# Performance work log

Hardware: AMD Instinct MI355X
Metric: run time of the kernel (lower is better)

Reference implementation:

```python
import jax, jax.numpy as jnp
import numpy as np

# ThrusterLagConfig constants
PWM_CENTER = 7.5
PWM_HALF_RANGE = 2.5
DEADZONE = 0.05
SAT_GAIN = 2.0
TAU_INIT = 0.08
TAU_MIN = 0.01
DT = 0.01
N_THRUSTERS = 8


def setup_inputs() -> dict:
    key = jax.random.key(0)
    k_u, = jax.random.split(key, 1)
    B, L, C = 512, 8192, N_THRUSTERS
    # raw PWM duty in [5, 10]
    u_seq = jax.random.uniform(k_u, (B, L, C), dtype=jnp.float32, minval=5.0, maxval=10.0)
    # learnable tau parameter, initialized as in __init__:
    # tau0 = clamp(tau_init - tau_min, 1e-6); p0 = log(expm1(tau0))
    tau0 = max(TAU_INIT - TAU_MIN, 1e-6)
    p0 = float(np.log(np.expm1(tau0)))
    tau_param = jnp.full((C,), p0, dtype=jnp.float32)
    return {"u_seq": u_seq, "tau_param": tau_param}


def reference(u_seq, tau_param):
    # PWM duty -> [-1, 1]
    u_unit = (u_seq - PWM_CENTER) / PWM_HALF_RANGE
    # deadzone: softshrink(u, lambd) = sign(u) * max(|u| - lambd, 0)
    u_dz = jnp.sign(u_unit) * jnp.maximum(jnp.abs(u_unit) - DEADZONE, 0.0)
    # smooth saturation
    u_nl = jnp.tanh(SAT_GAIN * u_dz)  # (B, L, C)

    # a = exp(-dt / tau), tau = softplus(p) + tau_min, per channel (C,)
    tau = jax.nn.softplus(tau_param) + TAU_MIN
    a = jnp.exp(-DT / tau)  # (C,)

    # first-order lag IIR: u_eff[k] = a * u_eff[k-1] + (1 - a) * u_nl[k]
    # u0_eff defaults to u_nl[:, 0, :]
    u0 = u_nl[:, 0, :]  # (B, C)

    def step(u_prev, uk):
        u_new = a * u_prev + (1.0 - a) * uk
        return u_new, u_new

    xs = jnp.moveaxis(u_nl, 1, 0)  # (L, B, C)
    _, ys = jax.lax.scan(step, u0, xs)
    return jnp.moveaxis(ys, 0, 1)  # (B, L, C)
```

## Files before the change

kernel.cpp:

```cpp
#include <hip/hip_runtime.h>
#include <math.h>


typedef float v4f __attribute__((ext_vector_type(4)));

constexpr int kB     = 512;
constexpr int kL     = 8192;
constexpr int kC     = 8;
constexpr int kOut   = 512;
constexpr int kChunk = 128;
constexpr int kSegs  = kL / kOut;

constexpr float kDT     = 0.01f;
constexpr float kTauMin = 0.01f;

__device__ __forceinline__ float rfl(float x) {
    return __int_as_float(__builtin_amdgcn_readfirstlane(__float_as_int(x)));
}

__device__ __forceinline__ float softplus_f(float p) {
    return fmaxf(p, 0.0f) + log1pf(__expf(-fabsf(p)));
}

__device__ __forceinline__ v4f u_nl4(v4f u) {
    v4f s = u * 0.8f - 6.0f;
    v4f x;
    #pragma unroll
    for (int i = 0; i < 4; ++i) {
        float cl = fminf(fmaxf(s[i], -0.1f), 0.1f);
        x[i] = s[i] - cl;
    }
    v4f t = x * x;
    v4f p = t * -0.0072811f + 0.070674f;
    p = t * p - 0.297221f;
    p = t * p + 0.996226f;
    return x * p;
}

template<int CTRL>
__device__ __forceinline__ float dpp_mov(float v) {
    return __int_as_float(__builtin_amdgcn_update_dpp(
        0, __float_as_int(v), CTRL, 0xF, 0xF, false));
}
#define DPP_SHR(d)   (0x110 | (d))
#define DPP_BC15     0x142
#define DPP_BC31     0x143

__device__ __forceinline__ float bperm(int addr, float v) {
    return __int_as_float(__builtin_amdgcn_ds_bpermute(addr, __float_as_int(v)));
}

#define PROC(X0, X1, X2, X3, CH, DO_PF, DO_ST)                                  \
    {                                                                           \
        v4f n0 = u_nl4(X0), n1 = u_nl4(X1), n2 = u_nl4(X2), n3 = u_nl4(X3);     \
        if (DO_PF) {                                                            \
            const float* nb = base +                                            \
                (size_t)(start + ((CH) + 2) * kChunk + lane * 2) * kC;          \
            X0 = *(const v4f*)(nb);                                             \
            X1 = *(const v4f*)(nb + 4);                                         \
            X2 = *(const v4f*)(nb + 8);                                         \
            X3 = *(const v4f*)(nb + 12);                                        \
        }                                                                       \
        v4f l00 = O0 * n0;                                                      \
        v4f l01 = O1 * n1;                                                      \
        v4f l10 = A0 * l00 + O0 * n2;                                           \
        v4f l11 = A1 * l01 + O1 * n3;                                           \
        float I[kC];                                                            \
        for (int c = 0; c < 4; ++c) { I[c] = l10[c]; I[c + 4] = l11[c]; }       \
        for (int c = 0; c < kC; ++c)                                            \
            I[c] = fmaf(a2[c], dpp_mov<DPP_SHR(1)>(I[c]), I[c]);                \
        for (int c = 0; c < kC; ++c)                                            \
            I[c] = fmaf(a4[c], dpp_mov<DPP_SHR(2)>(I[c]), I[c]);                \
        for (int c = 0; c < kC; ++c)                                            \
            I[c] = fmaf(a8[c], dpp_mov<DPP_SHR(4)>(I[c]), I[c]);                \
        for (int c = 0; c < kC; ++c)                                            \
            I[c] = fmaf(a16[c], dpp_mov<DPP_SHR(8)>(I[c]), I[c]);               \
        for (int c = 0; c < 4; ++c) {                                           \
            I[c]     = fmaf(W15a[c], dpp_mov<DPP_BC15>(I[c]),     I[c]);        \
            I[c + 4] = fmaf(W15b[c], dpp_mov<DPP_BC15>(I[c + 4]), I[c + 4]);    \
        }                                                                       \
        for (int c = 0; c < 4; ++c) {                                           \
            I[c]     = fmaf(W31a[c], dpp_mov<DPP_BC31>(I[c]),     I[c]);        \
            I[c + 4] = fmaf(W31b[c], dpp_mov<DPP_BC31>(I[c + 4]), I[c + 4]);    \
        }                                                                       \
        v4f Tt0, Tt1;                                                           \
        for (int c = 0; c < 4; ++c) {                                           \
            Tt0[c] = bperm(addr63, I[c]);                                       \
            Tt1[c] = bperm(addr63, I[c + 4]);                                   \
        }                                                                       \
        v4f I0 = {I[0], I[1], I[2], I[3]};                                      \
        v4f I1 = {I[4], I[5], I[6], I[7]};                                      \
        v4f E0 = (I0 - l10) * V0;                                               \
        v4f E1 = (I1 - l11) * V1;                                               \
        if (DO_ST) {                                                            \
            float* ob = obase +                                                 \
                (size_t)(start + (CH) * kChunk + lane * 2) * kC;                \
            v4f C0  = D0 * K0 + E0;                                             \
            v4f C1  = D1 * K1 + E1;                                             \
            v4f cy0 = A0 * C0;                                                  \
            v4f cy1 = A1 * C1;                                                  \
            *(v4f*)(ob)      = l00 + cy0;                                       \
            *(v4f*)(ob + 4)  = l01 + cy1;                                       \
            *(v4f*)(ob + 8)  = A0 * cy0 + l10;                                  \
            *(v4f*)(ob + 12) = A1 * cy1 + l11;                                  \
        }                                                                       \
        K0 = M0 * K0 + Tt0;                                                     \
        K1 = M1 * K1 + Tt1;                                                     \
    }

__global__ __launch_bounds__(256, 2) void scan_seg(const float* __restrict__ u,
                                                   const float* __restrict__ tp,
                                                   float* __restrict__ out) {
    const int lane = threadIdx.x & 63;
    const int seg  = blockIdx.x * 4 + (threadIdx.x >> 6);
    const int r    = seg >> 4;
    const int sq   = seg & (kSegs - 1);

    float a2[kC], a4[kC], a8[kC], a16[kC];
    float a[kC], om[kC], ia2[kC], Ms[kC];
    v4f D0, D1, W15a, W15b, W31a, W31b;
    #pragma unroll
    for (int c = 0; c < kC; ++c) {
        float tau = softplus_f(tp[c]) + kTauMin;
        float lna = -kDT / tau;
        float av  = __expf(lna);
        float v2 = av * av, v4 = v2 * v2, v8 = v4 * v4;
        a[c]   = rfl(av);
        om[c]  = rfl(1.0f - av);
        a2[c]  = rfl(v2);
        a4[c]  = rfl(v4);
        a8[c]  = rfl(v8);
        a16[c] = rfl(v8 * v8);
        ia2[c] = rfl(1.0f / v2);
        Ms[c]  = rfl(__expf(lna * (float)kChunk));
        float d   = __expf(lna * (float)(2 * lane));
        float w15 = (lane & 16)  ? __expf(lna * (float)(2 * ((lane & 15) + 1))) : 0.0f;
        float w31 = (lane >= 32) ? __expf(lna * (float)(2 * (lane - 31)))       : 0.0f;
        if (c < 4) { D0[c] = d; W15a[c] = w15; W31a[c] = w31; }
        else       { D1[c-4] = d; W15b[c-4] = w15; W31b[c-4] = w31; }
    }
    v4f A0 = {a[0],a[1],a[2],a[3]},     A1 = {a[4],a[5],a[6],a[7]};
    v4f O0 = {om[0],om[1],om[2],om[3]}, O1 = {om[4],om[5],om[6],om[7]};
    v4f V0 = {ia2[0],ia2[1],ia2[2],ia2[3]}, V1 = {ia2[4],ia2[5],ia2[6],ia2[7]};
    v4f M0 = {Ms[0],Ms[1],Ms[2],Ms[3]}, M1 = {Ms[4],Ms[5],Ms[6],Ms[7]};

    const float* base  = u   + (size_t)r * kL * kC;
    float*       obase = out + (size_t)r * kL * kC;

    const int addr63 = 63 << 2;

    v4f K0, K1;
    int start;
    if (sq == 0) {
        start = 0;
        K0 = u_nl4(*(const v4f*)(base));
        K1 = u_nl4(*(const v4f*)(base + 4));
    } else {
        start = sq * kOut - kChunk;
        K0 = (v4f){0, 0, 0, 0};
        K1 = (v4f){0, 0, 0, 0};
    }

    const float* pA = base + (size_t)(start + lane * 2) * kC;
    const float* pB = pA + (size_t)kChunk * kC;
    v4f xa0 = *(const v4f*)(pA);
    v4f xa1 = *(const v4f*)(pA + 4);
    v4f xa2 = *(const v4f*)(pA + 8);
    v4f xa3 = *(const v4f*)(pA + 12);
    v4f xb0 = *(const v4f*)(pB);
    v4f xb1 = *(const v4f*)(pB + 4);
    v4f xb2 = *(const v4f*)(pB + 8);
    v4f xb3 = *(const v4f*)(pB + 12);

    if (sq == 0) {
        PROC(xa0, xa1, xa2, xa3, 0, true,  true);
        PROC(xb0, xb1, xb2, xb3, 1, true,  true);
        PROC(xa0, xa1, xa2, xa3, 2, false, true);
        PROC(xb0, xb1, xb2, xb3, 3, false, true);
    } else {
        PROC(xa0, xa1, xa2, xa3, 0, true,  false);
        PROC(xb0, xb1, xb2, xb3, 1, true,  true);
        PROC(xa0, xa1, xa2, xa3, 2, true,  true);
        PROC(xb0, xb1, xb2, xb3, 3, false, true);
        PROC(xa0, xa1, xa2, xa3, 4, false, true);
    }
}

extern "C" void kernel_launch(void* const* d_in, const int* in_sizes, int n_in,
                              void* d_out, int out_size, void* d_ws, size_t ws_size,
                              hipStream_t stream) {
    const float* u  = (const float*)d_in[0];
    const float* tp = (const float*)d_in[1];
    float* out = (float*)d_out;

    scan_seg<<<(kB * kSegs) / 4, 256, 0, stream>>>(u, tp, out);
}
```

Before: 57.45 us.

## Software-pipeline chunk scans ahead of dependent stores and carry updates

Splits the per-chunk processing into a scan phase, a store phase and a carry-update phase. The scan of the next chunk is interleaved ahead of the previous chunk's store, so the DPP/bpermute scan work overlaps the serial carry chain. It also drops the launch_bounds occupancy hint. Keeping two chunks of intermediates live raises register pressure, and without the bound the compiler may pick lower occupancy.

```diff
diff --git a/kernel.cpp b/kernel.cpp
--- a/kernel.cpp
+++ b/kernel.cpp
@@ -50,23 +50,23 @@
     return __int_as_float(__builtin_amdgcn_ds_bpermute(addr, __float_as_int(v)));
 }
 
-#define PROC(X0, X1, X2, X3, CH, DO_PF, DO_ST)                                  \
+#define SCANM(l00v, l01v, l10v, l11v, E0v, E1v, T0v, T1v, X0, X1, X2, X3, DO_PF, PFCH) \
     {                                                                           \
         v4f n0 = u_nl4(X0), n1 = u_nl4(X1), n2 = u_nl4(X2), n3 = u_nl4(X3);     \
         if (DO_PF) {                                                            \
             const float* nb = base +                                            \
-                (size_t)(start + ((CH) + 2) * kChunk + lane * 2) * kC;          \
+                (size_t)(start + (PFCH) * kChunk + lane * 2) * kC;              \
             X0 = *(const v4f*)(nb);                                             \
             X1 = *(const v4f*)(nb + 4);                                         \
             X2 = *(const v4f*)(nb + 8);                                         \
             X3 = *(const v4f*)(nb + 12);                                        \
         }                                                                       \
-        v4f l00 = O0 * n0;                                                      \
-        v4f l01 = O1 * n1;                                                      \
-        v4f l10 = A0 * l00 + O0 * n2;                                           \
-        v4f l11 = A1 * l01 + O1 * n3;                                           \
+        l00v = O0 * n0;                                                         \
+        l01v = O1 * n1;                                                         \
+        l10v = A0 * l00v + O0 * n2;                                             \
+        l11v = A1 * l01v + O1 * n3;                                             \
         float I[kC];                                                            \
-        for (int c = 0; c < 4; ++c) { I[c] = l10[c]; I[c + 4] = l11[c]; }       \
+        for (int c = 0; c < 4; ++c) { I[c] = l10v[c]; I[c + 4] = l11v[c]; }     \
         for (int c = 0; c < kC; ++c)                                            \
             I[c] = fmaf(a2[c], dpp_mov<DPP_SHR(1)>(I[c]), I[c]);                \
         for (int c = 0; c < kC; ++c)                                            \
@@ -83,34 +83,34 @@
             I[c]     = fmaf(W31a[c], dpp_mov<DPP_BC31>(I[c]),     I[c]);        \
             I[c + 4] = fmaf(W31b[c], dpp_mov<DPP_BC31>(I[c + 4]), I[c + 4]);    \
         }                                                                       \
-        v4f Tt0, Tt1;                                                           \
         for (int c = 0; c < 4; ++c) {                                           \
-            Tt0[c] = bperm(addr63, I[c]);                                       \
-            Tt1[c] = bperm(addr63, I[c + 4]);                                   \
+            T0v[c] = bperm(addr63, I[c]);                                       \
+            T1v[c] = bperm(addr63, I[c + 4]);                                   \
         }                                                                       \
         v4f I0 = {I[0], I[1], I[2], I[3]};                                      \
         v4f I1 = {I[4], I[5], I[6], I[7]};                                      \
-        v4f E0 = (I0 - l10) * V0;                                               \
-        v4f E1 = (I1 - l11) * V1;                                               \
-        if (DO_ST) {                                                            \
-            float* ob = obase +                                                 \
-                (size_t)(start + (CH) * kChunk + lane * 2) * kC;                \
-            v4f C0  = D0 * K0 + E0;                                             \
-            v4f C1  = D1 * K1 + E1;                                             \
-            v4f cy0 = A0 * C0;                                                  \
-            v4f cy1 = A1 * C1;                                                  \
-            *(v4f*)(ob)      = l00 + cy0;                                       \
-            *(v4f*)(ob + 4)  = l01 + cy1;                                       \
-            *(v4f*)(ob + 8)  = A0 * cy0 + l10;                                  \
-            *(v4f*)(ob + 12) = A1 * cy1 + l11;                                  \
-        }                                                                       \
-        K0 = M0 * K0 + Tt0;                                                     \
-        K1 = M1 * K1 + Tt1;                                                     \
-    }
-
-__global__ __launch_bounds__(256, 2) void scan_seg(const float* __restrict__ u,
-                                                   const float* __restrict__ tp,
-                                                   float* __restrict__ out) {
+        E0v = (I0 - l10v) * V0;                                                 \
+        E1v = (I1 - l11v) * V1;                                                 \
+    }
+
+#define STOREM(l00v, l01v, l10v, l11v, E0v, E1v, CH)                            \
+    {                                                                           \
+        float* ob = obase + (size_t)(start + (CH) * kChunk + lane * 2) * kC;    \
+        v4f C0  = D0 * K0 + E0v;                                                \
+        v4f C1  = D1 * K1 + E1v;                                                \
+        v4f cy0 = A0 * C0;                                                      \
+        v4f cy1 = A1 * C1;                                                      \
+        *(v4f*)(ob)      = l00v + cy0;                                          \
+        *(v4f*)(ob + 4)  = l01v + cy1;                                          \
+        *(v4f*)(ob + 8)  = A0 * cy0 + l10v;                                     \
+        *(v4f*)(ob + 12) = A1 * cy1 + l11v;                                     \
+    }
+
+#define KUPD(T0v, T1v)  { K0 = M0 * K0 + T0v; K1 = M1 * K1 + T1v; }
+
+__global__ void scan_seg(const float* __restrict__ u,
+                         const float* __restrict__ tp,
+                         float* __restrict__ out) {
     const int lane = threadIdx.x & 63;
     const int seg  = blockIdx.x * 4 + (threadIdx.x >> 6);
     const int r    = seg >> 4;
@@ -172,17 +172,35 @@
     v4f xb2 = *(const v4f*)(pB + 8);
     v4f xb3 = *(const v4f*)(pB + 12);
 
+    v4f Al00, Al01, Al10, Al11, AE0, AE1, AT0, AT1;
+    v4f Bl00, Bl01, Bl10, Bl11, BE0, BE1, BT0, BT1;
+
     if (sq == 0) {
-        PROC(xa0, xa1, xa2, xa3, 0, true,  true);
-        PROC(xb0, xb1, xb2, xb3, 1, true,  true);
-        PROC(xa0, xa1, xa2, xa3, 2, false, true);
-        PROC(xb0, xb1, xb2, xb3, 3, false, true);
+        SCANM(Al00, Al01, Al10, Al11, AE0, AE1, AT0, AT1, xa0, xa1, xa2, xa3, true, 2);
+        SCANM(Bl00, Bl01, Bl10, Bl11, BE0, BE1, BT0, BT1, xb0, xb1, xb2, xb3, true, 3);
+        STOREM(Al00, Al01, Al10, Al11, AE0, AE1, 0);
+        KUPD(AT0, AT1);
+        SCANM(Al00, Al01, Al10, Al11, AE0, AE1, AT0, AT1, xa0, xa1, xa2, xa3, false, 0);
+        STOREM(Bl00, Bl01, Bl10, Bl11, BE0, BE1, 1);
+        KUPD(BT0, BT1);
+        SCANM(Bl00, Bl01, Bl10, Bl11, BE0, BE1, BT0, BT1, xb0, xb1, xb2, xb3, false, 0);
+        STOREM(Al00, Al01, Al10, Al11, AE0, AE1, 2);
+        KUPD(AT0, AT1);
+        STOREM(Bl00, Bl01, Bl10, Bl11, BE0, BE1, 3);
     } else {
-        PROC(xa0, xa1, xa2, xa3, 0, true,  false);
-        PROC(xb0, xb1, xb2, xb3, 1, true,  true);
-        PROC(xa0, xa1, xa2, xa3, 2, true,  true);
-        PROC(xb0, xb1, xb2, xb3, 3, false, true);
-        PROC(xa0, xa1, xa2, xa3, 4, false, true);
+        SCANM(Al00, Al01, Al10, Al11, AE0, AE1, AT0, AT1, xa0, xa1, xa2, xa3, true, 2);
+        SCANM(Bl00, Bl01, Bl10, Bl11, BE0, BE1, BT0, BT1, xb0, xb1, xb2, xb3, true, 3);
+        KUPD(AT0, AT1);
+        SCANM(Al00, Al01, Al10, Al11, AE0, AE1, AT0, AT1, xa0, xa1, xa2, xa3, true, 4);
+        STOREM(Bl00, Bl01, Bl10, Bl11, BE0, BE1, 1);
+        KUPD(BT0, BT1);
+        SCANM(Bl00, Bl01, Bl10, Bl11, BE0, BE1, BT0, BT1, xb0, xb1, xb2, xb3, false, 0);
+        STOREM(Al00, Al01, Al10, Al11, AE0, AE1, 2);
+        KUPD(AT0, AT1);
+        SCANM(Al00, Al01, Al10, Al11, AE0, AE1, AT0, AT1, xa0, xa1, xa2, xa3, false, 0);
+        STOREM(Bl00, Bl01, Bl10, Bl11, BE0, BE1, 3);
+        KUPD(BT0, BT1);
+        STOREM(Al00, Al01, Al10, Al11, AE0, AE1, 4);
     }
 }
 
```

Measured after the change: 116.4 us. 103% more time.
